# Optimization experiments

Measured on AMD Instinct MI355X. Metric: run time of the kernel, lower is better.

The kernel has to match this reference:

```python
import jax, jax.numpy as jnp
import numpy as np

B, T, P, I, H, C = 32, 64, 10, 1024, 1024, 8


def setup_inputs() -> dict:
    key = jax.random.key(0)
    ks = jax.random.split(key, 8)
    si = 1.0 / np.sqrt(I)
    sh = 1.0 / np.sqrt(H)
    return {
        "x":     jax.random.normal(ks[0], (B, T, P, I), dtype=jnp.float32),
        "Wx":    jax.random.normal(ks[1], (H, I), dtype=jnp.float32) * si,   # attention proj of person feats
        "Wh":    jax.random.normal(ks[2], (H, H), dtype=jnp.float32) * sh,   # attention proj of LSTM out
        "b_att": jnp.zeros((H,), dtype=jnp.float32),
        "v":     jax.random.normal(ks[3], (H,), dtype=jnp.float32) * sh,     # attention score vector
        "Wih":   jax.random.normal(ks[4], (4 * H, I), dtype=jnp.float32) * si,
        "Whh":   jax.random.normal(ks[5], (4 * H, H), dtype=jnp.float32) * sh,
        "bih":   jnp.zeros((4 * H,), dtype=jnp.float32),
        "bhh":   jnp.zeros((4 * H,), dtype=jnp.float32),
        "Wfc":   jax.random.normal(ks[6], (C, H), dtype=jnp.float32) * sh,
        "bfc":   jnp.zeros((C,), dtype=jnp.float32),
    }


def reference(x, Wx, Wh, b_att, v, Wih, Whh, bih, bhh, Wfc, bfc):
    b = x.shape[0]
    h_dim = Wh.shape[0]
    xt = jnp.transpose(x, (1, 0, 2, 3))  # (T,B,P,I) for scan over time

    def step(carry, x_t):
        out, h, c = carry  # each (B,H)
        # additive attention over persons, conditioned on previous LSTM output
        e = jnp.tanh(jnp.einsum('bpi,hi->bph', x_t, Wx) + (out @ Wh.T)[:, None, :] + b_att)
        alpha = jax.nn.softmax(e @ v, axis=-1)            # (B,P)
        emb = jnp.einsum('bp,bpi->bi', alpha, x_t)        # attention-pooled person features
        # single LSTM cell step (PyTorch gate order i,f,g,o)
        g = emb @ Wih.T + h @ Whh.T + bih + bhh           # (B,4H)
        i_, f_, g_, o_ = jnp.split(g, 4, axis=-1)
        c_new = jax.nn.sigmoid(f_) * c + jax.nn.sigmoid(i_) * jnp.tanh(g_)
        h_new = jax.nn.sigmoid(o_) * jnp.tanh(c_new)
        return (h_new, h_new, c_new), None

    z = jnp.zeros((b, h_dim), dtype=x.dtype)
    (out, _, _), _ = jax.lax.scan(step, (z, z, z), xt)
    return out @ Wfc.T + bfc  # (B,num_classes)
```

## Files before the change

kernel.cpp:

```cpp
#include <hip/hip_runtime.h>

#define BB 32
#define TT 64
#define PP 10
#define HH 1024
#define CC 8
#define MM 20480
#define NN 5120
#define KK 1024
#define NBLK 160
#define GEN_OFF (NBLK * 16)

typedef __attribute__((ext_vector_type(4))) float    f32x4;
typedef __attribute__((ext_vector_type(4))) _Float16 f16x4;
typedef __attribute__((ext_vector_type(8))) _Float16 f16x8;

#define AS1C(p) ((const __attribute__((address_space(1))) void*)(p))
#define AS3(p)  ((__attribute__((address_space(3))) void*)(p))

__device__ __forceinline__ float fast_tanh(float x) {
  float ax = __builtin_fabsf(x);
  float e  = __expf(2.0f * ax);
  float r  = 1.0f - 2.0f / (e + 1.0f);
  return __builtin_copysignf(r, x);
}
__device__ __forceinline__ float fast_sigm(float x) {
  return 1.0f / (1.0f + __expf(-x));
}

__device__ __forceinline__ int ld_flag(const int* p) {
  int r;
  asm volatile("global_load_dword %0, %1, off sc0 sc1\n\ts_waitcnt vmcnt(0)"
               : "=v"(r) : "v"(p) : "memory");
  return r;
}
__device__ __forceinline__ void st_flag(int* p, int v) {
  asm volatile("global_store_dword %0, %1, off sc0 sc1\n\ts_waitcnt vmcnt(0)"
               :: "v"(p), "v"(v) : "memory");
}
__device__ __forceinline__ void st_f32_sc(float* p, float v) {
  asm volatile("global_store_dword %0, %1, off sc0 sc1" :: "v"(p), "v"(v) : "memory");
}
__device__ __forceinline__ void st_u32_sc(unsigned* p, unsigned v) {
  asm volatile("global_store_dword %0, %1, off sc0 sc1" :: "v"(p), "v"(v) : "memory");
}
__device__ __forceinline__ void st_u16_sc(unsigned short* p, unsigned v) {
  asm volatile("global_store_short %0, %1, off sc0 sc1" :: "v"(p), "v"(v) : "memory");
}
__device__ __forceinline__ f32x4 ld_f32x4_sc(const float* p) {
  f32x4 r;
  asm volatile("global_load_dwordx4 %0, %1, off sc0 sc1\n\ts_waitcnt vmcnt(0)"
               : "=v"(r) : "v"(p) : "memory");
  return r;
}
__device__ __forceinline__ void load_a8_sc(
    const _Float16* p0, const _Float16* p1, const _Float16* p2, const _Float16* p3,
    const _Float16* p4, const _Float16* p5, const _Float16* p6, const _Float16* p7,
    f16x8& d0, f16x8& d1, f16x8& d2, f16x8& d3,
    f16x8& d4, f16x8& d5, f16x8& d6, f16x8& d7)
{
  asm volatile(
    "global_load_dwordx4 %0, %8, off sc0 sc1\n\t"
    "global_load_dwordx4 %1, %9, off sc0 sc1\n\t"
    "global_load_dwordx4 %2, %10, off sc0 sc1\n\t"
    "global_load_dwordx4 %3, %11, off sc0 sc1\n\t"
    "global_load_dwordx4 %4, %12, off sc0 sc1\n\t"
    "global_load_dwordx4 %5, %13, off sc0 sc1\n\t"
    "global_load_dwordx4 %6, %14, off sc0 sc1\n\t"
    "global_load_dwordx4 %7, %15, off sc0 sc1\n\t"
    "s_waitcnt vmcnt(0)"
    : "=v"(d0), "=v"(d1), "=v"(d2), "=v"(d3), "=v"(d4), "=v"(d5), "=v"(d6), "=v"(d7)
    : "v"(p0), "v"(p1), "v"(p2), "v"(p3), "v"(p4), "v"(p5), "v"(p6), "v"(p7)
    : "memory");
}
__device__ __forceinline__ void ld_att_gates_sc(
    const float* pa, const float* pb,
    const float* q0, const float* q1, const float* q2, const float* q3,
    const float* q4, const float* q5, const float* q6, const float* q7,
    f32x4& ra, f32x4& rb,
    float& r0, float& r1, float& r2, float& r3,
    float& r4, float& r5, float& r6, float& r7)
{
  asm volatile(
    "global_load_dwordx4 %0, %10, off sc0 sc1\n\t"
    "global_load_dwordx4 %1, %11, off sc0 sc1\n\t"
    "global_load_dword %2, %12, off sc0 sc1\n\t"
    "global_load_dword %3, %13, off sc0 sc1\n\t"
    "global_load_dword %4, %14, off sc0 sc1\n\t"
    "global_load_dword %5, %15, off sc0 sc1\n\t"
    "global_load_dword %6, %16, off sc0 sc1\n\t"
    "global_load_dword %7, %17, off sc0 sc1\n\t"
    "global_load_dword %8, %18, off sc0 sc1\n\t"
    "global_load_dword %9, %19, off sc0 sc1\n\t"
    "s_waitcnt vmcnt(0)"
    : "=v"(ra), "=v"(rb), "=v"(r0), "=v"(r1), "=v"(r2), "=v"(r3),
      "=v"(r4), "=v"(r5), "=v"(r6), "=v"(r7)
    : "v"(pa), "v"(pb), "v"(q0), "v"(q1), "v"(q2), "v"(q3),
      "v"(q4), "v"(q5), "v"(q6), "v"(q7)
    : "memory");
}

__global__ void convert_kernel(const float* __restrict__ x,
                               const float* __restrict__ Wx,
                               const float* __restrict__ Wih,
                               const float* __restrict__ Wh,
                               const float* __restrict__ Whh,
                               _Float16* __restrict__ xh,
                               _Float16* __restrict__ w5,
                               _Float16* __restrict__ w2)
{
  const long gid    = (long)blockIdx.x * blockDim.x + threadIdx.x;
  const long stride = (long)gridDim.x * blockDim.x;
  auto cvt = [&](const float* src, _Float16* dst, long n4) {
    const f32x4* s4 = (const f32x4*)src;
    f16x4* d4 = (f16x4*)dst;
    for (long i = gid; i < n4; i += stride)
      d4[i] = __builtin_convertvector(s4[i], f16x4);
  };
  cvt(x,   xh,                 (long)MM * KK / 4);
  cvt(Wx,  w5,                 (long)HH * KK / 4);
  cvt(Wih, w5 + (long)HH * KK, (long)4 * HH * KK / 4);
  cvt(Wh,  w2,                 (long)HH * KK / 4);
  cvt(Whh, w2 + (long)HH * KK, (long)4 * HH * KK / 4);
}

__global__ __launch_bounds__(256) void gemm_kernel(const _Float16* __restrict__ A,
                                                   const _Float16* __restrict__ Bw,
                                                   _Float16* __restrict__ Cw)
{
  __shared__ __align__(16) _Float16 sA[128 * 64];
  __shared__ __align__(16) _Float16 sB[128 * 64];
  const int t    = threadIdx.x;
  const int lane = t & 63;
  const int wave = t >> 6;
  const int wm = wave >> 1, wn = wave & 1;
  const int q = lane >> 4, cl = lane & 15;

  const int gid   = blockIdx.x;
  const int panel = gid / 640;
  const int w     = gid % 640;
  const int bm = panel * 16 + (w & 15);
  const int bn = w >> 4;

  const _Float16* Ag = A  + (size_t)bm * 128 * KK;
  const _Float16* Bg = Bw + (size_t)bn * 128 * KK;

  f32x4 acc[4][4];
#pragma unroll
  for (int mi = 0; mi < 4; mi++)
#pragma unroll
    for (int ni = 0; ni < 4; ni++)
      acc[mi][ni] = (f32x4){0.f, 0.f, 0.f, 0.f};

  for (int k0 = 0; k0 < KK; k0 += 64) {
#pragma unroll
    for (int i = 0; i < 4; i++) {
      int c = t + 256 * i;
      int row = c >> 3, col8 = c & 7;
      __builtin_amdgcn_global_load_lds(AS1C(Ag + (size_t)row * KK + k0 + col8 * 8),
                                       AS3(sA + c * 8), 16, 0, 0);
      __builtin_amdgcn_global_load_lds(AS1C(Bg + (size_t)row * KK + k0 + col8 * 8),
                                       AS3(sB + c * 8), 16, 0, 0);
    }
    __syncthreads();
#pragma unroll
    for (int ks = 0; ks < 2; ks++) {
      f16x8 af[4], bf[4];
#pragma unroll
      for (int mi = 0; mi < 4; mi++)
        af[mi] = *(const f16x8*)(sA + (wm * 64 + mi * 16 + cl) * 64 + ks * 32 + q * 8);
#pragma unroll
      for (int ni = 0; ni < 4; ni++)
        bf[ni] = *(const f16x8*)(sB + (wn * 64 + ni * 16 + cl) * 64 + ks * 32 + q * 8);
#pragma unroll
      for (int mi = 0; mi < 4; mi++)
#pragma unroll
        for (int ni = 0; ni < 4; ni++)
          acc[mi][ni] = __builtin_amdgcn_mfma_f32_16x16x32_f16(af[mi], bf[ni], acc[mi][ni], 0, 0, 0);
    }
    __syncthreads();
  }

#pragma unroll
  for (int mi = 0; mi < 4; mi++)
#pragma unroll
    for (int ni = 0; ni < 4; ni++)
#pragma unroll
      for (int r = 0; r < 4; r++) {
        int row = bm * 128 + wm * 64 + mi * 16 + q * 4 + r;
        int col = bn * 128 + wn * 64 + ni * 16 + cl;
        Cw[(size_t)row * NN + col] = (_Float16)acc[mi][ni][r];
      }
}

__device__ __forceinline__ void grid_barrier(int* flags, int ph) {
  asm volatile("s_waitcnt vmcnt(0)" ::: "memory");
  __syncthreads();
  if (blockIdx.x == 0) {
    const int tid = threadIdx.x;
    if (tid >= 1 && tid < NBLK)
      while (ld_flag(flags + tid * 16) < ph) {}
    __syncthreads();
    if (tid == 0) st_flag(flags + GEN_OFF, ph);
  } else {
    if (threadIdx.x == 0) {
      st_flag(flags + blockIdx.x * 16, ph);
      while (ld_flag(flags + GEN_OFF) < ph) {}
    }
  }
  __syncthreads();
}

__global__ __launch_bounds__(256) void recur_kernel(
    const _Float16* __restrict__ xw,
    const _Float16* __restrict__ w2,
    float* __restrict__ a5a,
    float* __restrict__ a5b,
    float* __restrict__ h,
    _Float16* __restrict__ h16,
    int* __restrict__ flags,
    const float* __restrict__ b_att,
    const float* __restrict__ v,
    const float* __restrict__ bih,
    const float* __restrict__ bhh,
    const float* __restrict__ Wfc,
    const float* __restrict__ bfc,
    float* __restrict__ out)
{
  const int tid  = threadIdx.x;
  const int bid  = blockIdx.x;
  const int lane = tid & 63;
  const int wave = tid >> 6;
  const int q = lane >> 4, cl = lane & 15;

  __shared__ float red[4][PP];
  __shared__ float alpha_s[PP];

  int ph = 0;

  const int job = bid * 4 + wave;
  const int nt  = job >> 1;
  const int kh  = job & 1;
  const _Float16* Bb = w2 + (size_t)(nt * 16 + cl) * KK + kh * 512 + q * 8;
  f16x8 breg[16];
#pragma unroll
  for (int ks = 0; ks < 16; ks++)
    breg[ks] = *(const f16x8*)(Bb + ks * 32);

  if (bid < BB) {
    unsigned* p = (unsigned*)(h16 + (size_t)bid * HH);
    st_u32_sc(p + tid, 0u);
    st_u32_sc(p + 256 + tid, 0u);
  }
  float c_reg = 0.f;

  grid_barrier(flags, ++ph);

  for (int t = 0; t < TT; ++t) {
    {
      const _Float16* A0 = h16 + (size_t)cl * KK + kh * 512 + q * 8;
      const _Float16* A1 = A0 + (size_t)16 * KK;
      f32x4 acc0 = {0.f, 0.f, 0.f, 0.f}, acc1 = {0.f, 0.f, 0.f, 0.f};
#pragma unroll
      for (int g = 0; g < 4; g++) {
        f16x8 a0[4], a1[4];
        load_a8_sc(A0 + (g * 4 + 0) * 32, A0 + (g * 4 + 1) * 32,
                   A0 + (g * 4 + 2) * 32, A0 + (g * 4 + 3) * 32,
                   A1 + (g * 4 + 0) * 32, A1 + (g * 4 + 1) * 32,
                   A1 + (g * 4 + 2) * 32, A1 + (g * 4 + 3) * 32,
                   a0[0], a0[1], a0[2], a0[3], a1[0], a1[1], a1[2], a1[3]);
#pragma unroll
        for (int j = 0; j < 4; j++) {
          acc0 = __builtin_amdgcn_mfma_f32_16x16x32_f16(a0[j], breg[g * 4 + j], acc0, 0, 0, 0);
          acc1 = __builtin_amdgcn_mfma_f32_16x16x32_f16(a1[j], breg[g * 4 + j], acc1, 0, 0, 0);
        }
      }
      float* a5w = kh ? a5b : a5a;
#pragma unroll
      for (int r = 0; r < 4; r++) {
        st_f32_sc(a5w + (size_t)(q * 4 + r) * NN + nt * 16 + cl,      acc0[r]);
        st_f32_sc(a5w + (size_t)(16 + q * 4 + r) * NN + nt * 16 + cl, acc1[r]);
      }
    }
    grid_barrier(flags, ++ph);

    if (bid < 128) {
      const int b  = bid & 31;
      const int us = bid >> 5;
      const int u  = us * 256 + tid;
      const size_t rbase = ((size_t)b * TT + t) * PP;

      f16x4 xv[PP];
#pragma unroll
      for (int p = 0; p < PP; p++)
        xv[p] = ((const f16x4*)(xw + (rbase + p) * NN))[tid];
      _Float16 xg[4][PP];
#pragma unroll
      for (int gi = 0; gi < 4; gi++)
#pragma unroll
        for (int p = 0; p < PP; p++)
          xg[gi][p] = xw[(rbase + p) * NN + HH + gi * HH + u];

      const float* pa = a5a + (size_t)b * NN + 4 * tid;
      const float* pb = a5b + (size_t)b * NN + 4 * tid;
      const float* g0a = a5a + (size_t)b * NN + HH + u;
      const float* g0b = a5b + (size_t)b * NN + HH + u;
      f32x4 va, vb;
      float ga0, ga1, ga2, ga3, gb0, gb1, gb2, gb3;
      ld_att_gates_sc(pa, pb,
                      g0a, g0a + HH, g0a + 2 * HH, g0a + 3 * HH,
                      g0b, g0b + HH, g0b + 2 * HH, g0b + 3 * HH,
                      va, vb, ga0, ga1, ga2, ga3, gb0, gb1, gb2, gb3);

      f32x4 vv = ((const f32x4*)v)[tid];
      f32x4 aa = va + vb + ((const f32x4*)b_att)[tid];
      float part[PP];
#pragma unroll
      for (int p = 0; p < PP; p++) {
        f32x4 xf = __builtin_convertvector(xv[p], f32x4);
        float s = 0.f;
#pragma unroll
        for (int j = 0; j < 4; j++)
          s += vv[j] * fast_tanh(aa[j] + xf[j]);
        part[p] = s;
      }
#pragma unroll
      for (int p = 0; p < PP; p++) {
        float s = part[p];
        s += __shfl_down(s, 32); s += __shfl_down(s, 16); s += __shfl_down(s, 8);
        s += __shfl_down(s, 4);  s += __shfl_down(s, 2);  s += __shfl_down(s, 1);
        if (lane == 0) red[wave][p] = s;
      }
      __syncthreads();
      if (tid == 0) {
        float sc[PP]; float mx = -1e30f;
#pragma unroll
        for (int p = 0; p < PP; p++) {
          sc[p] = red[0][p] + red[1][p] + red[2][p] + red[3][p];
          mx = fmaxf(mx, sc[p]);
        }
        float den = 0.f;
#pragma unroll
        for (int p = 0; p < PP; p++) { sc[p] = __expf(sc[p] - mx); den += sc[p]; }
        float inv = 1.0f / den;
#pragma unroll
        for (int p = 0; p < PP; p++) alpha_s[p] = sc[p] * inv;
      }
      __syncthreads();
      float al[PP];
#pragma unroll
      for (int p = 0; p < PP; p++) al[p] = alpha_s[p];

      float gsum[4] = {ga0 + gb0, ga1 + gb1, ga2 + gb2, ga3 + gb3};
      float gv[4];
#pragma unroll
      for (int gi = 0; gi < 4; gi++) {
        float s = gsum[gi] + bih[gi * HH + u] + bhh[gi * HH + u];
#pragma unroll
        for (int p = 0; p < PP; p++)
          s += al[p] * (float)xg[gi][p];
        gv[gi] = s;
      }
      float ig = fast_sigm(gv[0]);
      float fg = fast_sigm(gv[1]);
      float gg = fast_tanh(gv[2]);
      float og = fast_sigm(gv[3]);
      float cn = fg * c_reg + ig * gg;
      float hn = og * fast_tanh(cn);
      c_reg = cn;
      _Float16 h16v = (_Float16)hn;
      st_u16_sc((unsigned short*)(h16 + (size_t)b * HH + u),
                (unsigned)__builtin_bit_cast(unsigned short, h16v));
      if (t == TT - 1)
        st_f32_sc(h + (size_t)b * HH + u, hn);
    }
    grid_barrier(flags, ++ph);
  }

  if (bid < BB) {
    const int b = bid;
    f32x4 hv = ld_f32x4_sc(h + (size_t)b * HH + 4 * tid);
    float pc[CC];
#pragma unroll
    for (int cc2 = 0; cc2 < CC; cc2++) {
      f32x4 wv = ((const f32x4*)(Wfc + (size_t)cc2 * HH))[tid];
      pc[cc2] = hv[0]*wv[0] + hv[1]*wv[1] + hv[2]*wv[2] + hv[3]*wv[3];
    }
#pragma unroll
    for (int cc2 = 0; cc2 < CC; cc2++) {
      float s = pc[cc2];
      s += __shfl_down(s, 32); s += __shfl_down(s, 16); s += __shfl_down(s, 8);
      s += __shfl_down(s, 4);  s += __shfl_down(s, 2);  s += __shfl_down(s, 1);
      if (lane == 0) red[wave][cc2] = s;
    }
    __syncthreads();
    if (tid < CC)
      out[b * CC + tid] = red[0][tid] + red[1][tid] + red[2][tid] + red[3][tid] + bfc[tid];
  }
}

extern "C" void kernel_launch(void* const* d_in, const int* in_sizes, int n_in,
                              void* d_out, int out_size, void* d_ws, size_t ws_size,
                              hipStream_t stream)
{
  (void)in_sizes; (void)n_in; (void)out_size; (void)ws_size;
  const float* x     = (const float*)d_in[0];
  const float* Wx    = (const float*)d_in[1];
  const float* Wh    = (const float*)d_in[2];
  const float* b_att = (const float*)d_in[3];
  const float* v     = (const float*)d_in[4];
  const float* Wih   = (const float*)d_in[5];
  const float* Whh   = (const float*)d_in[6];
  const float* bih   = (const float*)d_in[7];
  const float* bhh   = (const float*)d_in[8];
  const float* Wfc   = (const float*)d_in[9];
  const float* bfc   = (const float*)d_in[10];
  float* out = (float*)d_out;

  char* ws = (char*)d_ws;
  size_t off = 0;
  auto alloc = [&](size_t bytes) {
    size_t o = off;
    off += (bytes + 255) & ~(size_t)255;
    return o;
  };
  int*      flags = (int*)      (ws + alloc(16384));
  _Float16* xh    = (_Float16*) (ws + alloc((size_t)MM * KK * 2));
  _Float16* w5    = (_Float16*) (ws + alloc((size_t)NN * KK * 2));
  _Float16* w2    = (_Float16*) (ws + alloc((size_t)NN * KK * 2));
  _Float16* xw    = (_Float16*) (ws + alloc((size_t)MM * NN * 2));
  float*    a5a   = (float*)    (ws + alloc((size_t)BB * NN * 4));
  float*    a5b   = (float*)    (ws + alloc((size_t)BB * NN * 4));
  float*    h     = (float*)    (ws + alloc((size_t)BB * HH * 4));
  _Float16* h16   = (_Float16*) (ws + alloc((size_t)BB * HH * 2));

  hipMemsetAsync(flags, 0, 16384, stream);
  convert_kernel<<<2048, 256, 0, stream>>>(x, Wx, Wih, Wh, Whh, xh, w5, w2);
  gemm_kernel<<<6400, 256, 0, stream>>>(xh, w5, xw);
  recur_kernel<<<NBLK, 256, 0, stream>>>(xw, w2, a5a, a5b, h, h16, flags,
                                         b_att, v, bih, bhh, Wfc, bfc, out);
}
```

Baseline: 1.397 ms.

## Split recurrent kernel into producer/consumer block roles with point-to-point flags

```diff
diff --git a/kernel.cpp b/kernel.cpp
--- a/kernel.cpp
+++ b/kernel.cpp
@@ -8,8 +8,9 @@
 #define MM 20480
 #define NN 5120
 #define KK 1024
-#define NBLK 160
-#define GEN_OFF (NBLK * 16)
+#define RBLK 128
+#define GBLK 80
+#define GRID (RBLK + GBLK)
 
 typedef __attribute__((ext_vector_type(4))) float    f32x4;
 typedef __attribute__((ext_vector_type(4))) _Float16 f16x4;
@@ -35,8 +36,7 @@
   return r;
 }
 __device__ __forceinline__ void st_flag(int* p, int v) {
-  asm volatile("global_store_dword %0, %1, off sc0 sc1\n\ts_waitcnt vmcnt(0)"
-               :: "v"(p), "v"(v) : "memory");
+  asm volatile("global_store_dword %0, %1, off sc0 sc1" :: "v"(p), "v"(v) : "memory");
 }
 __device__ __forceinline__ void st_f32_sc(float* p, float v) {
   asm volatile("global_store_dword %0, %1, off sc0 sc1" :: "v"(p), "v"(v) : "memory");
@@ -53,7 +53,11 @@
                : "=v"(r) : "v"(p) : "memory");
   return r;
 }
-__device__ __forceinline__ void load_a8_sc(
+__device__ __forceinline__ void vm_drain() {
+  asm volatile("s_waitcnt vmcnt(0)" ::: "memory");
+}
+
+__device__ __forceinline__ void load8_nw(
     const _Float16* p0, const _Float16* p1, const _Float16* p2, const _Float16* p3,
     const _Float16* p4, const _Float16* p5, const _Float16* p6, const _Float16* p7,
     f16x8& d0, f16x8& d1, f16x8& d2, f16x8& d3,
@@ -67,11 +71,24 @@
     "global_load_dwordx4 %4, %12, off sc0 sc1\n\t"
     "global_load_dwordx4 %5, %13, off sc0 sc1\n\t"
     "global_load_dwordx4 %6, %14, off sc0 sc1\n\t"
-    "global_load_dwordx4 %7, %15, off sc0 sc1\n\t"
-    "s_waitcnt vmcnt(0)"
+    "global_load_dwordx4 %7, %15, off sc0 sc1"
     : "=v"(d0), "=v"(d1), "=v"(d2), "=v"(d3), "=v"(d4), "=v"(d5), "=v"(d6), "=v"(d7)
     : "v"(p0), "v"(p1), "v"(p2), "v"(p3), "v"(p4), "v"(p5), "v"(p6), "v"(p7)
     : "memory");
+}
+__device__ __forceinline__ void wait_vm8_tie(
+    f16x8& d0, f16x8& d1, f16x8& d2, f16x8& d3,
+    f16x8& d4, f16x8& d5, f16x8& d6, f16x8& d7)
+{
+  asm volatile("s_waitcnt vmcnt(8)"
+    : "+v"(d0), "+v"(d1), "+v"(d2), "+v"(d3), "+v"(d4), "+v"(d5), "+v"(d6), "+v"(d7));
+}
+__device__ __forceinline__ void wait_vm0_tie(
+    f16x8& d0, f16x8& d1, f16x8& d2, f16x8& d3,
+    f16x8& d4, f16x8& d5, f16x8& d6, f16x8& d7)
+{
+  asm volatile("s_waitcnt vmcnt(0)"
+    : "+v"(d0), "+v"(d1), "+v"(d2), "+v"(d3), "+v"(d4), "+v"(d5), "+v"(d6), "+v"(d7));
 }
 __device__ __forceinline__ void ld_att_gates_sc(
     const float* pa, const float* pb,
@@ -193,25 +210,7 @@
       }
 }
 
-__device__ __forceinline__ void grid_barrier(int* flags, int ph) {
-  asm volatile("s_waitcnt vmcnt(0)" ::: "memory");
-  __syncthreads();
-  if (blockIdx.x == 0) {
-    const int tid = threadIdx.x;
-    if (tid >= 1 && tid < NBLK)
-      while (ld_flag(flags + tid * 16) < ph) {}
-    __syncthreads();
-    if (tid == 0) st_flag(flags + GEN_OFF, ph);
-  } else {
-    if (threadIdx.x == 0) {
-      st_flag(flags + blockIdx.x * 16, ph);
-      while (ld_flag(flags + GEN_OFF) < ph) {}
-    }
-  }
-  __syncthreads();
-}
-
-__global__ __launch_bounds__(256) void recur_kernel(
+__global__ __launch_bounds__(256, 1) void recur_kernel(
     const _Float16* __restrict__ xw,
     const _Float16* __restrict__ w2,
     float* __restrict__ a5a,
@@ -236,150 +235,204 @@
   __shared__ float red[4][PP];
   __shared__ float alpha_s[PP];
 
-  int ph = 0;
-
-  const int job = bid * 4 + wave;
-  const int nt  = job >> 1;
-  const int kh  = job & 1;
-  const _Float16* Bb = w2 + (size_t)(nt * 16 + cl) * KK + kh * 512 + q * 8;
-  f16x8 breg[16];
-#pragma unroll
-  for (int ks = 0; ks < 16; ks++)
-    breg[ks] = *(const f16x8*)(Bb + ks * 32);
+  if (bid >= RBLK) {
+    const int job  = (bid - RBLK) * 4 + wave;
+    const int ngrp = job >> 1;
+    const int kh   = job & 1;
+    const int nt0  = ngrp * 2, nt1 = nt0 + 1;
+
+    f16x8 breg[2][16];
+#pragma unroll
+    for (int j = 0; j < 2; j++)
+#pragma unroll
+      for (int ks = 0; ks < 16; ks++)
+        breg[j][ks] = *(const f16x8*)(w2 + (size_t)((nt0 + j) * 16 + cl) * KK
+                                      + kh * 512 + ks * 32 + q * 8);
+
+    float* a5w = kh ? a5b : a5a;
+    const _Float16* A0 = h16 + (size_t)cl * KK + kh * 512 + q * 8;
+    const _Float16* A1 = A0 + (size_t)16 * KK;
+
+    for (int t = 0; t < TT; ++t) {
+      if (tid < RBLK)
+        while (ld_flag(flags + tid * 16) < t + 1) {}
+      __syncthreads();
+
+      f32x4 acc00 = {0,0,0,0}, acc10 = {0,0,0,0}, acc01 = {0,0,0,0}, acc11 = {0,0,0,0};
+      f16x8 w0[8], w1[8], w2r[8], w3[8];
+      load8_nw(A0 + 0*32, A0 + 1*32, A0 + 2*32, A0 + 3*32,
+               A0 + 4*32, A0 + 5*32, A0 + 6*32, A0 + 7*32,
+               w0[0], w0[1], w0[2], w0[3], w0[4], w0[5], w0[6], w0[7]);
+      load8_nw(A0 + 8*32, A0 + 9*32, A0 + 10*32, A0 + 11*32,
+               A0 + 12*32, A0 + 13*32, A0 + 14*32, A0 + 15*32,
+               w1[0], w1[1], w1[2], w1[3], w1[4], w1[5], w1[6], w1[7]);
+      wait_vm8_tie(w0[0], w0[1], w0[2], w0[3], w0[4], w0[5], w0[6], w0[7]);
+#pragma unroll
+      for (int ks = 0; ks < 8; ks++) {
+        acc00 = __builtin_amdgcn_mfma_f32_16x16x32_f16(w0[ks], breg[0][ks], acc00, 0, 0, 0);
+        acc10 = __builtin_amdgcn_mfma_f32_16x16x32_f16(w0[ks], breg[1][ks], acc10, 0, 0, 0);
+      }
+      load8_nw(A1 + 0*32, A1 + 1*32, A1 + 2*32, A1 + 3*32,
+               A1 + 4*32, A1 + 5*32, A1 + 6*32, A1 + 7*32,
+               w2r[0], w2r[1], w2r[2], w2r[3], w2r[4], w2r[5], w2r[6], w2r[7]);
+      wait_vm8_tie(w1[0], w1[1], w1[2], w1[3], w1[4], w1[5], w1[6], w1[7]);
+#pragma unroll
+      for (int ks = 0; ks < 8; ks++) {
+        acc00 = __builtin_amdgcn_mfma_f32_16x16x32_f16(w1[ks], breg[0][8 + ks], acc00, 0, 0, 0);
+        acc10 = __builtin_amdgcn_mfma_f32_16x16x32_f16(w1[ks], breg[1][8 + ks], acc10, 0, 0, 0);
+      }
+      load8_nw(A1 + 8*32, A1 + 9*32, A1 + 10*32, A1 + 11*32,
+               A1 + 12*32, A1 + 13*32, A1 + 14*32, A1 + 15*32,
+               w3[0], w3[1], w3[2], w3[3], w3[4], w3[5], w3[6], w3[7]);
+      wait_vm8_tie(w2r[0], w2r[1], w2r[2], w2r[3], w2r[4], w2r[5], w2r[6], w2r[7]);
+#pragma unroll
+      for (int ks = 0; ks < 8; ks++) {
+        acc01 = __builtin_amdgcn_mfma_f32_16x16x32_f16(w2r[ks], breg[0][ks], acc01, 0, 0, 0);
+        acc11 = __builtin_amdgcn_mfma_f32_16x16x32_f16(w2r[ks], breg[1][ks], acc11, 0, 0, 0);
+      }
+      wait_vm0_tie(w3[0], w3[1], w3[2], w3[3], w3[4], w3[5], w3[6], w3[7]);
+#pragma unroll
+      for (int ks = 0; ks < 8; ks++) {
+        acc01 = __builtin_amdgcn_mfma_f32_16x16x32_f16(w3[ks], breg[0][8 + ks], acc01, 0, 0, 0);
+        acc11 = __builtin_amdgcn_mfma_f32_16x16x32_f16(w3[ks], breg[1][8 + ks], acc11, 0, 0, 0);
+      }
+#pragma unroll
+      for (int r = 0; r < 4; r++) {
+        st_f32_sc(a5w + (size_t)(q * 4 + r) * NN + nt0 * 16 + cl,      acc00[r]);
+        st_f32_sc(a5w + (size_t)(q * 4 + r) * NN + nt1 * 16 + cl,      acc10[r]);
+        st_f32_sc(a5w + (size_t)(16 + q * 4 + r) * NN + nt0 * 16 + cl, acc01[r]);
+        st_f32_sc(a5w + (size_t)(16 + q * 4 + r) * NN + nt1 * 16 + cl, acc11[r]);
+      }
+      vm_drain();
+      __syncthreads();
+      if (tid == 0) st_flag(flags + bid * 16, t + 1);
+      __syncthreads();
+    }
+    return;
+  }
+
+  const int b  = bid & 31;
+  const int us = bid >> 5;
+  const int u  = us * 256 + tid;
 
   if (bid < BB) {
     unsigned* p = (unsigned*)(h16 + (size_t)bid * HH);
     st_u32_sc(p + tid, 0u);
     st_u32_sc(p + 256 + tid, 0u);
   }
+  vm_drain();
+  __syncthreads();
+  if (tid == 0) st_flag(flags + bid * 16, 1);
+
+  f32x4 vv   = ((const f32x4*)v)[tid];
+  f32x4 batt = ((const f32x4*)b_att)[tid];
+  float bsum[4];
+#pragma unroll
+  for (int gi = 0; gi < 4; gi++)
+    bsum[gi] = bih[gi * HH + u] + bhh[gi * HH + u];
   float c_reg = 0.f;
 
-  grid_barrier(flags, ++ph);
-
   for (int t = 0; t < TT; ++t) {
-    {
-      const _Float16* A0 = h16 + (size_t)cl * KK + kh * 512 + q * 8;
-      const _Float16* A1 = A0 + (size_t)16 * KK;
-      f32x4 acc0 = {0.f, 0.f, 0.f, 0.f}, acc1 = {0.f, 0.f, 0.f, 0.f};
-#pragma unroll
-      for (int g = 0; g < 4; g++) {
-        f16x8 a0[4], a1[4];
-        load_a8_sc(A0 + (g * 4 + 0) * 32, A0 + (g * 4 + 1) * 32,
-                   A0 + (g * 4 + 2) * 32, A0 + (g * 4 + 3) * 32,
-                   A1 + (g * 4 + 0) * 32, A1 + (g * 4 + 1) * 32,
-                   A1 + (g * 4 + 2) * 32, A1 + (g * 4 + 3) * 32,
-                   a0[0], a0[1], a0[2], a0[3], a1[0], a1[1], a1[2], a1[3]);
-#pragma unroll
-        for (int j = 0; j < 4; j++) {
-          acc0 = __builtin_amdgcn_mfma_f32_16x16x32_f16(a0[j], breg[g * 4 + j], acc0, 0, 0, 0);
-          acc1 = __builtin_amdgcn_mfma_f32_16x16x32_f16(a1[j], breg[g * 4 + j], acc1, 0, 0, 0);
-        }
-      }
-      float* a5w = kh ? a5b : a5a;
-#pragma unroll
-      for (int r = 0; r < 4; r++) {
-        st_f32_sc(a5w + (size_t)(q * 4 + r) * NN + nt * 16 + cl,      acc0[r]);
-        st_f32_sc(a5w + (size_t)(16 + q * 4 + r) * NN + nt * 16 + cl, acc1[r]);
-      }
-    }
-    grid_barrier(flags, ++ph);
-
-    if (bid < 128) {
-      const int b  = bid & 31;
-      const int us = bid >> 5;
-      const int u  = us * 256 + tid;
-      const size_t rbase = ((size_t)b * TT + t) * PP;
-
-      f16x4 xv[PP];
+    const size_t rbase = ((size_t)b * TT + t) * PP;
+
+    f16x4 xv[PP];
+#pragma unroll
+    for (int p = 0; p < PP; p++)
+      xv[p] = ((const f16x4*)(xw + (rbase + p) * NN))[tid];
+    _Float16 xg[4][PP];
+#pragma unroll
+    for (int gi = 0; gi < 4; gi++)
 #pragma unroll
       for (int p = 0; p < PP; p++)
-        xv[p] = ((const f16x4*)(xw + (rbase + p) * NN))[tid];
-      _Float16 xg[4][PP];
-#pragma unroll
-      for (int gi = 0; gi < 4; gi++)
-#pragma unroll
-        for (int p = 0; p < PP; p++)
-          xg[gi][p] = xw[(rbase + p) * NN + HH + gi * HH + u];
-
-      const float* pa = a5a + (size_t)b * NN + 4 * tid;
-      const float* pb = a5b + (size_t)b * NN + 4 * tid;
-      const float* g0a = a5a + (size_t)b * NN + HH + u;
-      const float* g0b = a5b + (size_t)b * NN + HH + u;
-      f32x4 va, vb;
-      float ga0, ga1, ga2, ga3, gb0, gb1, gb2, gb3;
-      ld_att_gates_sc(pa, pb,
-                      g0a, g0a + HH, g0a + 2 * HH, g0a + 3 * HH,
-                      g0b, g0b + HH, g0b + 2 * HH, g0b + 3 * HH,
-                      va, vb, ga0, ga1, ga2, ga3, gb0, gb1, gb2, gb3);
-
-      f32x4 vv = ((const f32x4*)v)[tid];
-      f32x4 aa = va + vb + ((const f32x4*)b_att)[tid];
-      float part[PP];
+        xg[gi][p] = xw[(rbase + p) * NN + HH + gi * HH + u];
+
+    if (tid < GBLK)
+      while (ld_flag(flags + (RBLK + tid) * 16) < t + 1) {}
+    __syncthreads();
+
+    const float* pa  = a5a + (size_t)b * NN + 4 * tid;
+    const float* pb  = a5b + (size_t)b * NN + 4 * tid;
+    const float* g0a = a5a + (size_t)b * NN + HH + u;
+    const float* g0b = a5b + (size_t)b * NN + HH + u;
+    f32x4 va, vb;
+    float ga0, ga1, ga2, ga3, gb0, gb1, gb2, gb3;
+    ld_att_gates_sc(pa, pb,
+                    g0a, g0a + HH, g0a + 2 * HH, g0a + 3 * HH,
+                    g0b, g0b + HH, g0b + 2 * HH, g0b + 3 * HH,
+                    va, vb, ga0, ga1, ga2, ga3, gb0, gb1, gb2, gb3);
+
+    f32x4 aa = va + vb + batt;
+    float part[PP];
+#pragma unroll
+    for (int p = 0; p < PP; p++) {
+      f32x4 xf = __builtin_convertvector(xv[p], f32x4);
+      float s = 0.f;
+#pragma unroll
+      for (int j = 0; j < 4; j++)
+        s += vv[j] * fast_tanh(aa[j] + xf[j]);
+      part[p] = s;
+    }
+#pragma unroll
+    for (int p = 0; p < PP; p++) {
+      float s = part[p];
+      s += __shfl_down(s, 32); s += __shfl_down(s, 16); s += __shfl_down(s, 8);
+      s += __shfl_down(s, 4);  s += __shfl_down(s, 2);  s += __shfl_down(s, 1);
+      if (lane == 0) red[wave][p] = s;
+    }
+    __syncthreads();
+    if (tid == 0) {
+      float sc[PP]; float mx = -1e30f;
 #pragma unroll
       for (int p = 0; p < PP; p++) {
-        f32x4 xf = __builtin_convertvector(xv[p], f32x4);
-        float s = 0.f;
-#pragma unroll
-        for (int j = 0; j < 4; j++)
-          s += vv[j] * fast_tanh(aa[j] + xf[j]);
-        part[p] = s;
-      }
-#pragma unroll
-      for (int p = 0; p < PP; p++) {
-        float s = part[p];
-        s += __shfl_down(s, 32); s += __shfl_down(s, 16); s += __shfl_down(s, 8);
-        s += __shfl_down(s, 4);  s += __shfl_down(s, 2);  s += __shfl_down(s, 1);
-        if (lane == 0) red[wave][p] = s;
-      }
-      __syncthreads();
-      if (tid == 0) {
-        float sc[PP]; float mx = -1e30f;
-#pragma unroll
-        for (int p = 0; p < PP; p++) {
-          sc[p] = red[0][p] + red[1][p] + red[2][p] + red[3][p];
-          mx = fmaxf(mx, sc[p]);
-        }
-        float den = 0.f;
-#pragma unroll
-        for (int p = 0; p < PP; p++) { sc[p] = __expf(sc[p] - mx); den += sc[p]; }
-        float inv = 1.0f / den;
-#pragma unroll
-        for (int p = 0; p < PP; p++) alpha_s[p] = sc[p] * inv;
-      }
-      __syncthreads();
-      float al[PP];
-#pragma unroll
-      for (int p = 0; p < PP; p++) al[p] = alpha_s[p];
-
-      float gsum[4] = {ga0 + gb0, ga1 + gb1, ga2 + gb2, ga3 + gb3};
-      float gv[4];
-#pragma unroll
-      for (int gi = 0; gi < 4; gi++) {
-        float s = gsum[gi] + bih[gi * HH + u] + bhh[gi * HH + u];
-#pragma unroll
-        for (int p = 0; p < PP; p++)
-          s += al[p] * (float)xg[gi][p];
-        gv[gi] = s;
-      }
-      float ig = fast_sigm(gv[0]);
-      float fg = fast_sigm(gv[1]);
-      float gg = fast_tanh(gv[2]);
-      float og = fast_sigm(gv[3]);
-      float cn = fg * c_reg + ig * gg;
-      float hn = og * fast_tanh(cn);
-      c_reg = cn;
-      _Float16 h16v = (_Float16)hn;
-      st_u16_sc((unsigned short*)(h16 + (size_t)b * HH + u),
-                (unsigned)__builtin_bit_cast(unsigned short, h16v));
-      if (t == TT - 1)
-        st_f32_sc(h + (size_t)b * HH + u, hn);
-    }
-    grid_barrier(flags, ++ph);
+        sc[p] = red[0][p] + red[1][p] + red[2][p] + red[3][p];
+        mx = fmaxf(mx, sc[p]);
+      }
+      float den = 0.f;
+#pragma unroll
+      for (int p = 0; p < PP; p++) { sc[p] = __expf(sc[p] - mx); den += sc[p]; }
+      float inv = 1.0f / den;
+#pragma unroll
+      for (int p = 0; p < PP; p++) alpha_s[p] = sc[p] * inv;
+    }
+    __syncthreads();
+    float al[PP];
+#pragma unroll
+    for (int p = 0; p < PP; p++) al[p] = alpha_s[p];
+
+    float gsum[4] = {ga0 + gb0, ga1 + gb1, ga2 + gb2, ga3 + gb3};
+    float gv[4];
+#pragma unroll
+    for (int gi = 0; gi < 4; gi++) {
+      float s = gsum[gi] + bsum[gi];
+#pragma unroll
+      for (int p = 0; p < PP; p++)
+        s += al[p] * (float)xg[gi][p];
+      gv[gi] = s;
+    }
+    float ig = fast_sigm(gv[0]);
+    float fg = fast_sigm(gv[1]);
+    float gg = fast_tanh(gv[2]);
+    float og = fast_sigm(gv[3]);
+    float cn = fg * c_reg + ig * gg;
+    float hn = og * fast_tanh(cn);
+    c_reg = cn;
+    _Float16 h16v = (_Float16)hn;
+    st_u16_sc((unsigned short*)(h16 + (size_t)b * HH + u),
+              (unsigned)__builtin_bit_cast(unsigned short, h16v));
+    if (t == TT - 1)
+      st_f32_sc(h + (size_t)b * HH + u, hn);
+
+    vm_drain();
+    __syncthreads();
+    if (tid == 0) st_flag(flags + bid * 16, t + 2);
+    __syncthreads();
   }
 
   if (bid < BB) {
-    const int b = bid;
-    f32x4 hv = ld_f32x4_sc(h + (size_t)b * HH + 4 * tid);
+    if (tid >= 1 && tid <= 3)
+      while (ld_flag(flags + (bid + 32 * tid) * 16) < TT + 1) {}
+    __syncthreads();
+    f32x4 hv = ld_f32x4_sc(h + (size_t)bid * HH + 4 * tid);
     float pc[CC];
 #pragma unroll
     for (int cc2 = 0; cc2 < CC; cc2++) {
@@ -395,7 +448,7 @@
     }
     __syncthreads();
     if (tid < CC)
-      out[b * CC + tid] = red[0][tid] + red[1][tid] + red[2][tid] + red[3][tid] + bfc[tid];
+      out[bid * CC + tid] = red[0][tid] + red[1][tid] + red[2][tid] + red[3][tid] + bfc[tid];
   }
 }
 
@@ -424,7 +477,7 @@
     off += (bytes + 255) & ~(size_t)255;
     return o;
   };
-  int*      flags = (int*)      (ws + alloc(16384));
+  int*      flags = (int*)      (ws + alloc(65536));
   _Float16* xh    = (_Float16*) (ws + alloc((size_t)MM * KK * 2));
   _Float16* w5    = (_Float16*) (ws + alloc((size_t)NN * KK * 2));
   _Float16* w2    = (_Float16*) (ws + alloc((size_t)NN * KK * 2));
@@ -434,9 +487,9 @@
   float*    h     = (float*)    (ws + alloc((size_t)BB * HH * 4));
   _Float16* h16   = (_Float16*) (ws + alloc((size_t)BB * HH * 2));
 
-  hipMemsetAsync(flags, 0, 16384, stream);
+  hipMemsetAsync(flags, 0, 65536, stream);
   convert_kernel<<<2048, 256, 0, stream>>>(x, Wx, Wih, Wh, Whh, xh, w5, w2);
   gemm_kernel<<<6400, 256, 0, stream>>>(xh, w5, xw);
-  recur_kernel<<<NBLK, 256, 0, stream>>>(xw, w2, a5a, a5b, h, h16, flags,
+  recur_kernel<<<GRID, 256, 0, stream>>>(xw, w2, a5a, a5b, h, h16, flags,
                                          b_att, v, bih, bhh, Wfc, bfc, out);
 }
```

Measured after the change: 1.251 ms. -10.4%, faster.
